# Kernel tuning notes

Hardware: AMD Instinct MI355X
Metric: run time of the kernel (lower is better)

The kernel has to match this reference:

```python
import jax, jax.numpy as jnp
import numpy as np

DIM = 384
HEADS = 12
WS = 7
MLPH = 1536
B = 32
EPS = 1e-5


def _rel_index():
    coords = np.stack(np.meshgrid(np.arange(WS), np.arange(WS), indexing='ij'))  # [2,7,7]
    cf = coords.reshape(2, -1)  # [2,49]
    rel = cf[:, :, None] - cf[:, None, :]  # [2,49,49]
    rel = rel.transpose(1, 2, 0).astype(np.int64)
    rel[:, :, 0] += WS - 1
    rel[:, :, 1] += WS - 1
    rel[:, :, 0] *= 2 * WS - 1
    return jnp.asarray(rel.sum(-1), dtype=jnp.int32)  # [49,49]


def setup_inputs() -> dict:
    key = jax.random.key(0)
    ks = jax.random.split(key, 16)
    H, W = 56, 56
    L = H * W
    s = 0.02
    inp = {
        'x': jax.random.normal(ks[0], (B, L, DIM), jnp.float32),
        'ln1_g': jnp.ones((DIM,), jnp.float32),
        'ln1_b': jnp.zeros((DIM,), jnp.float32),
        'qkv_w': jax.random.normal(ks[1], (DIM, 3 * DIM), jnp.float32) * s,
        'qkv_b': jnp.zeros((3 * DIM,), jnp.float32),
        'rpb_table': jax.random.normal(ks[2], ((2 * WS - 1) ** 2, HEADS), jnp.float32) * s,
        'proj_w': jax.random.normal(ks[3], (DIM, DIM), jnp.float32) * s,
        'proj_b': jnp.zeros((DIM,), jnp.float32),
        'ln2_g': jnp.ones((DIM,), jnp.float32),
        'ln2_b': jnp.zeros((DIM,), jnp.float32),
        'mlp_w1': jax.random.normal(ks[4], (DIM, MLPH), jnp.float32) * s,
        'mlp_b1': jnp.zeros((MLPH,), jnp.float32),
        'mlp_w2': jax.random.normal(ks[5], (MLPH, DIM), jnp.float32) * s,
        'mlp_b2': jnp.zeros((DIM,), jnp.float32),
        'rel_idx': _rel_index(),
        'H': H,
        'W': W,
    }
    return inp


def _ln(x, g, b):
    m = jnp.mean(x, axis=-1, keepdims=True)
    v = jnp.mean(jnp.square(x - m), axis=-1, keepdims=True)
    return (x - m) * jax.lax.rsqrt(v + EPS) * g + b


def reference(x, ln1_g, ln1_b, qkv_w, qkv_b, rpb_table, proj_w, proj_b,
              ln2_g, ln2_b, mlp_w1, mlp_b1, mlp_w2, mlp_b2, rel_idx, H, W):
    Bb, L, C = x.shape
    N = WS * WS
    hd = C // HEADS
    scale = hd ** -0.5

    shortcut = x
    h = _ln(x, ln1_g, ln1_b).reshape(Bb, H, W, C)
    # window partition -> [nW, 49, C]
    h = h.reshape(Bb, H // WS, WS, W // WS, WS, C).transpose(0, 1, 3, 2, 4, 5)
    wins = h.reshape(-1, N, C)
    nW = wins.shape[0]

    qkv = (wins @ qkv_w + qkv_b).reshape(nW, N, 3, HEADS, hd).transpose(2, 0, 3, 1, 4)
    q, k, v = qkv[0] * scale, qkv[1], qkv[2]  # [nW, heads, 49, hd]

    attn = jnp.einsum('bhnd,bhmd->bhnm', q, k)
    bias = rpb_table[rel_idx].transpose(2, 0, 1)  # [heads,49,49]
    attn = jax.nn.softmax(attn + bias[None], axis=-1)
    out = jnp.einsum('bhnm,bhmd->bhnd', attn, v).transpose(0, 2, 1, 3).reshape(nW, N, C)
    out = out @ proj_w + proj_b

    # window reverse -> [B, L, C]
    out = out.reshape(Bb, H // WS, W // WS, WS, WS, C).transpose(0, 1, 3, 2, 4, 5).reshape(Bb, L, C)

    x = shortcut + out
    h2 = _ln(x, ln2_g, ln2_b)
    mlp = jax.nn.gelu(h2 @ mlp_w1 + mlp_b1, approximate=False) @ mlp_w2 + mlp_b2
    return x + mlp
```

## Files before the change

### kernel.cpp

```cpp
#include <hip/hip_runtime.h>
#include <hip/hip_bf16.h>
#include <cstdint>
#include <cstddef>

#define HEADS 12
#define LL 3136
#define ROWS 100352
#define SCALE 0.17677669529663687f

typedef __hip_bfloat16 bf16;
typedef __attribute__((ext_vector_type(8))) short short8;
typedef __attribute__((ext_vector_type(4))) short s4;
typedef __attribute__((ext_vector_type(4))) float f32x4;

__device__ __forceinline__ float bf2f(unsigned short u) {
  union { uint32_t u32; float f; } x; x.u32 = ((uint32_t)u) << 16; return x.f;
}
__device__ __forceinline__ unsigned short f2bf_bits(float f) {
  union { float f; uint32_t u; } x; x.f = f;
  uint32_t r = x.u + 0x7fffu + ((x.u >> 16) & 1u);
  return (unsigned short)(r >> 16);
}
__device__ __forceinline__ float gelu_fast(float x) {
  float t2 = x * (1.5957691216f + 0.0713548162726f * x * x);
  float e = __expf(t2);
  return x * (e / (e + 1.0f));
}

__global__ __launch_bounds__(64) void prep_fragB(const float* __restrict__ src,
    bf16* __restrict__ dst, int K, int N, int scaleLim, float scale) {
  const int nf = blockIdx.x, kf = blockIdx.y;
  const int l = threadIdx.x;
  const int n = nf * 16 + (l & 15);
  const int k0 = kf * 32 + (l >> 4) * 8;
  const float sc = (n < scaleLim) ? scale : 1.f;
  short8 v;
  #pragma unroll
  for (int j = 0; j < 8; ++j)
    v[j] = (short)f2bf_bits(src[(size_t)(k0 + j) * N + n] * sc);
  *(short8*)&dst[(((size_t)nf * (K >> 5) + kf) * 64 + l) * 8] = v;
}

__global__ void prep_qb(const float* __restrict__ qkv_b, float* __restrict__ qb) {
  int idx = blockIdx.x * 256 + threadIdx.x;
  if (idx < 1152) qb[idx] = qkv_b[idx] * (idx < 384 ? SCALE : 1.0f);
}

__global__ void prep_biasM(const float* __restrict__ rpb, const int* __restrict__ rel,
                           f32x4* __restrict__ biasM) {
  int h = blockIdx.x;
  int t = blockIdx.y;
  int mi = t >> 2, ni = t & 3;
  int lane = threadIdx.x;
  int q = ni * 16 + (lane & 15);
  int g = lane >> 4;
  f32x4 v;
  #pragma unroll
  for (int j = 0; j < 4; ++j) {
    int k = mi * 16 + g * 4 + j;
    float b;
    if (k < 49) b = (q < 49) ? rpb[rel[q * 49 + k] * HEADS + h] : 0.f;
    else        b = -1e30f;
    v[j] = b;
  }
  biasM[((h * 4 + mi) * 4 + ni) * 64 + lane] = v;
}

template<bool WIN, bool BF16IN>
__global__ __launch_bounds__(256) void ln_kernel(const float* __restrict__ xf,
    const bf16* __restrict__ xb, const float* __restrict__ g,
    const float* __restrict__ b, bf16* __restrict__ out) {
  int row = blockIdx.x * 4 + (threadIdx.x >> 6);
  int lane = threadIdx.x & 63;
  size_t src;
  if (WIN) {
    int w = row / 49, p = row - w * 49;
    int bb = w >> 6, wy = (w >> 3) & 7, wx = w & 7;
    int iy = p / 7, ix = p - iy * 7;
    int l = (wy * 7 + iy) * 56 + wx * 7 + ix;
    src = ((size_t)bb * LL + l) * 384;
  } else {
    src = (size_t)row * 384;
  }
  float vals[6];
  float s = 0.f, s2 = 0.f;
  #pragma unroll
  for (int j = 0; j < 6; ++j) {
    float v = BF16IN ? bf2f(*(const unsigned short*)&xb[src + lane + 64 * j])
                     : xf[src + lane + 64 * j];
    vals[j] = v; s += v; s2 += v * v;
  }
  #pragma unroll
  for (int off = 32; off >= 1; off >>= 1) {
    s  += __shfl_xor(s, off);
    s2 += __shfl_xor(s2, off);
  }
  float m  = s * (1.f / 384.f);
  float var = s2 * (1.f / 384.f) - m * m;
  float rs = rsqrtf(var + 1e-5f);
  bf16* orow = out + (size_t)row * 384;
  #pragma unroll
  for (int j = 0; j < 6; ++j) {
    int c = lane + 64 * j;
    orow[c] = __float2bfloat16((vals[j] - m) * rs * g[c] + b[c]);
  }
}

template<int EPI, int KTOT>
__global__ __launch_bounds__(256) void gemm_bt(const bf16* __restrict__ A,
    const bf16* __restrict__ Bt, const float* __restrict__ bias,
    bf16* __restrict__ Cb, float* __restrict__ Cf, const float* __restrict__ resid,
    const bf16* __restrict__ residb, int M, int N) {
  constexpr int KC  = 384;
  constexpr int NCH = KTOT / KC;
  constexpr int NT  = KC / 32;
  constexpr int NKF = KTOT >> 5;
  __shared__ bf16 lsA[128 * KC];
  const int t = threadIdx.x;
  const int lane = t & 63;
  const int wave = t >> 6;
  const int wm = wave >> 1, wn = wave & 1;
  const int lrow = lane & 15;
  const int lk = (lane >> 4) * 8;
  const int nbx = N >> 7;
  const int nwg = (M >> 7) * nbx;
  const int cpx = nwg >> 3;
  const int id2 = (blockIdx.x & 7) * cpx + (blockIdx.x >> 3);
  const int n0 = (id2 % nbx) * 128;
  const int m0 = (id2 / nbx) * 128;

  f32x4 acc[4][4];
  #pragma unroll
  for (int i = 0; i < 4; ++i)
    #pragma unroll
    for (int j = 0; j < 4; ++j) acc[i][j] = (f32x4){0.f, 0.f, 0.f, 0.f};

  for (int kc = 0; kc < NCH; ++kc) {
    if (kc) __syncthreads();
    #pragma unroll
    for (int tt = 0; tt < NT; ++tt) {
      #pragma unroll
      for (int i = 0; i < 2; ++i) {
        int e = (i * 256 + t) * 8;
        int r = e >> 5, c = e & 31;
        const bf16* ga = A + (size_t)(m0 + r) * KTOT + kc * KC + tt * 32 + c;
        __builtin_amdgcn_global_load_lds((const __attribute__((address_space(1))) void*)ga,
            (__attribute__((address_space(3))) void*)&lsA[tt * 4096 + e], 16, 0, 0);
      }
    }
    __syncthreads();
    #pragma unroll
    for (int tt = 0; tt < NT; ++tt) {
      const int kf = kc * NT + tt;
      short8 bfr[4];
      const bf16* fb = Bt + (((size_t)((n0 >> 4) + wn * 4) * NKF + kf) * 64 + lane) * 8;
      #pragma unroll
      for (int ni = 0; ni < 4; ++ni)
        bfr[ni] = *(const short8*)(fb + (size_t)ni * NKF * 512);
      short8 af[4];
      #pragma unroll
      for (int mi = 0; mi < 4; ++mi)
        af[mi] = *(const short8*)&lsA[tt * 4096 + (wm * 64 + mi * 16 + lrow) * 32 + lk];
      #pragma unroll
      for (int mi = 0; mi < 4; ++mi)
        #pragma unroll
        for (int ni = 0; ni < 4; ++ni)
          acc[mi][ni] = __builtin_amdgcn_mfma_f32_16x16x32_bf16(af[mi], bfr[ni], acc[mi][ni], 0, 0, 0);
    }
  }

  #pragma unroll
  for (int mi = 0; mi < 4; ++mi) {
    #pragma unroll
    for (int ni = 0; ni < 4; ++ni) {
      int col = n0 + wn * 64 + ni * 16 + lrow;
      float bv = bias[col];
      #pragma unroll
      for (int j = 0; j < 4; ++j) {
        int row = m0 + wm * 64 + mi * 16 + (lane >> 4) * 4 + j;
        float v = acc[mi][ni][j] + bv;
        if constexpr (EPI == 0) {
          Cb[(size_t)row * N + col] = __float2bfloat16(v);
        } else if constexpr (EPI == 1) {
          Cb[(size_t)row * N + col] = __float2bfloat16(gelu_fast(v));
        } else if constexpr (EPI == 2) {
          int w = row / 49, p = row - w * 49;
          int bb = w >> 6, wy = (w >> 3) & 7, wx = w & 7;
          int iy = p / 7, ix = p - iy * 7;
          int l = (wy * 7 + iy) * 56 + wx * 7 + ix;
          size_t di = ((size_t)bb * LL + l) * 384 + col;
          Cb[di] = __float2bfloat16(v + resid[di]);
        } else {
          size_t di = (size_t)row * N + col;
          Cf[di] = v + bf2f(*(const unsigned short*)&residb[di]);
        }
      }
    }
  }
}

__global__ __launch_bounds__(256) void attn_mfma(const bf16* __restrict__ qkv,
    const f32x4* __restrict__ biasM, bf16* __restrict__ out) {
  __shared__ __align__(16) short lds4[4][6272];
  const int wv = threadIdx.x >> 6;
  const int lane = threadIdx.x & 63;
  const int w = blockIdx.x * 4 + wv;
  const int h = blockIdx.y;
  short* L = &lds4[wv][0];
  const short* base = (const short*)(qkv + (size_t)w * 49 * 1152 + h * 32);

  #pragma unroll
  for (int i = 0; i < 4; ++i) {
    int t = i * 64 + lane;
    int r = t >> 2, c = t & 3;
    short8 qv, kv, vv;
    if (r < 49) {
      const short* rp = base + (size_t)r * 1152;
      qv = *(const short8*)(rp + c * 8);
      kv = *(const short8*)(rp + 384 + c * 8);
      vv = *(const short8*)(rp + 768 + c * 8);
    } else {
      qv = (short8)0; kv = (short8)0; vv = (short8)0;
    }
    *(short8*)&L[r * 32 + c * 8] = kv;
    *(short8*)&L[2048 + r * 32 + c * 8] = qv;
    #pragma unroll
    for (int j = 0; j < 8; ++j) L[4096 + (c * 8 + j) * 68 + r] = vv[j];
  }

  const int g = lane >> 4, r15 = lane & 15;

  short8 ka[4], qb[4];
  #pragma unroll
  for (int mi = 0; mi < 4; ++mi)
    ka[mi] = *(const short8*)&L[(mi * 16 + r15) * 32 + g * 8];
  #pragma unroll
  for (int ni = 0; ni < 4; ++ni)
    qb[ni] = *(const short8*)&L[2048 + (ni * 16 + r15) * 32 + g * 8];

  f32x4 sT[4][4];
  #pragma unroll
  for (int mi = 0; mi < 4; ++mi)
    #pragma unroll
    for (int ni = 0; ni < 4; ++ni)
      sT[mi][ni] = biasM[((h * 4 + mi) * 4 + ni) * 64 + lane];
  #pragma unroll
  for (int mi = 0; mi < 4; ++mi)
    #pragma unroll
    for (int ni = 0; ni < 4; ++ni)
      sT[mi][ni] = __builtin_amdgcn_mfma_f32_16x16x32_bf16(ka[mi], qb[ni], sT[mi][ni], 0, 0, 0);

  float inv_[4];
  #pragma unroll
  for (int ni = 0; ni < 4; ++ni) {
    float m = -1e30f;
    #pragma unroll
    for (int mi = 0; mi < 4; ++mi)
      #pragma unroll
      for (int j = 0; j < 4; ++j) m = fmaxf(m, sT[mi][ni][j]);
    m = fmaxf(m, __shfl_xor(m, 16));
    m = fmaxf(m, __shfl_xor(m, 32));
    float s = 0.f;
    #pragma unroll
    for (int mi = 0; mi < 4; ++mi)
      #pragma unroll
      for (int j = 0; j < 4; ++j) {
        float p = __expf(sT[mi][ni][j] - m);
        sT[mi][ni][j] = p; s += p;
      }
    s += __shfl_xor(s, 16);
    s += __shfl_xor(s, 32);
    inv_[ni] = 1.f / s;
  }

  s4 pa[4][4];
  #pragma unroll
  for (int mi = 0; mi < 4; ++mi)
    #pragma unroll
    for (int ni = 0; ni < 4; ++ni) {
      s4 p;
      #pragma unroll
      for (int j = 0; j < 4; ++j)
        p[j] = (short)f2bf_bits(sT[mi][ni][j] * inv_[ni]);
      pa[mi][ni] = p;
    }

  s4 vb[4][2];
  #pragma unroll
  for (int mi = 0; mi < 4; ++mi)
    #pragma unroll
    for (int di = 0; di < 2; ++di)
      vb[mi][di] = *(const s4*)&L[4096 + (di * 16 + r15) * 68 + mi * 16 + g * 4];

  f32x4 o[4][2];
  #pragma unroll
  for (int ni = 0; ni < 4; ++ni)
    #pragma unroll
    for (int di = 0; di < 2; ++di) o[ni][di] = (f32x4){0.f, 0.f, 0.f, 0.f};

  asm volatile("s_nop 3" ::: );
  #pragma unroll
  for (int ni = 0; ni < 4; ++ni)
    #pragma unroll
    for (int di = 0; di < 2; ++di)
      #pragma unroll
      for (int mi = 0; mi < 4; ++mi) {
#if __has_builtin(__builtin_amdgcn_mfma_f32_16x16x16bf16_1k)
        o[ni][di] = __builtin_amdgcn_mfma_f32_16x16x16bf16_1k(pa[mi][ni], vb[mi][di], o[ni][di], 0, 0, 0);
#else
        asm volatile("v_mfma_f32_16x16x16_bf16 %0, %1, %2, %0"
                     : "+v"(o[ni][di]) : "v"(pa[mi][ni]), "v"(vb[mi][di]));
#endif
      }
  asm volatile("s_nop 7\n\ts_nop 7" ::: );

  bf16* op = out + ((size_t)w * 49) * 384 + h * 32;
  #pragma unroll
  for (int ni = 0; ni < 4; ++ni)
    #pragma unroll
    for (int di = 0; di < 2; ++di)
      #pragma unroll
      for (int j = 0; j < 4; ++j) {
        int q = ni * 16 + g * 4 + j;
        if (q < 49)
          op[(size_t)q * 384 + di * 16 + r15] = __float2bfloat16(o[ni][di][j]);
      }
}

extern "C" void kernel_launch(void* const* d_in, const int* in_sizes, int n_in,
                              void* d_out, int out_size, void* d_ws, size_t ws_size,
                              hipStream_t stream) {
  const float* x      = (const float*)d_in[0];
  const float* ln1_g  = (const float*)d_in[1];
  const float* ln1_b  = (const float*)d_in[2];
  const float* qkv_w  = (const float*)d_in[3];
  const float* qkv_b  = (const float*)d_in[4];
  const float* rpb    = (const float*)d_in[5];
  const float* proj_w = (const float*)d_in[6];
  const float* proj_b = (const float*)d_in[7];
  const float* ln2_g  = (const float*)d_in[8];
  const float* ln2_b  = (const float*)d_in[9];
  const float* mlp_w1 = (const float*)d_in[10];
  const float* mlp_b1 = (const float*)d_in[11];
  const float* mlp_w2 = (const float*)d_in[12];
  const float* mlp_b2 = (const float*)d_in[13];
  const int*   rel    = (const int*)d_in[14];

  char* ws = (char*)d_ws;
  const size_t OFF_WQKV  = 0;
  const size_t OFF_WPROJ = OFF_WQKV + (size_t)1152 * 384 * 2;
  const size_t OFF_WM1   = OFF_WPROJ + (size_t)384 * 384 * 2;
  const size_t OFF_WM2   = OFF_WM1 + (size_t)1536 * 384 * 2;
  const size_t OFF_QB    = OFF_WM2 + (size_t)384 * 1536 * 2;
  const size_t OFF_HWIN  = 3659776;
  const size_t OFF_QKV   = OFF_HWIN + (size_t)ROWS * 384 * 2;
  const size_t OFF_ATTN  = OFF_QKV + (size_t)ROWS * 1152 * 2;
  const size_t OFF_X2    = OFF_ATTN + (size_t)ROWS * 384 * 2;
  const size_t OFF_M1    = OFF_QKV;
  const size_t OFF_H2    = OFF_HWIN;
  const size_t OFF_BIASM = OFF_X2 + (size_t)ROWS * 384 * 2;

  bf16*  wqkv  = (bf16*)(ws + OFF_WQKV);
  bf16*  wproj = (bf16*)(ws + OFF_WPROJ);
  bf16*  wm1   = (bf16*)(ws + OFF_WM1);
  bf16*  wm2   = (bf16*)(ws + OFF_WM2);
  float* qb    = (float*)(ws + OFF_QB);
  f32x4* biasM = (f32x4*)(ws + OFF_BIASM);
  bf16*  hwin  = (bf16*)(ws + OFF_HWIN);
  bf16*  qkvb  = (bf16*)(ws + OFF_QKV);
  bf16*  attnb = (bf16*)(ws + OFF_ATTN);
  bf16*  x2b   = (bf16*)(ws + OFF_X2);
  bf16*  m1    = (bf16*)(ws + OFF_M1);
  bf16*  h2    = (bf16*)(ws + OFF_H2);
  float* outp  = (float*)d_out;

  prep_fragB<<<dim3(1152 / 16, 384 / 32), 64, 0, stream>>>(qkv_w, wqkv, 384, 1152, 384, SCALE);
  prep_fragB<<<dim3(384 / 16, 384 / 32), 64, 0, stream>>>(proj_w, wproj, 384, 384, 0, 1.f);
  prep_fragB<<<dim3(1536 / 16, 384 / 32), 64, 0, stream>>>(mlp_w1, wm1, 384, 1536, 0, 1.f);
  prep_fragB<<<dim3(384 / 16, 1536 / 32), 64, 0, stream>>>(mlp_w2, wm2, 1536, 384, 0, 1.f);
  prep_qb<<<5, 256, 0, stream>>>(qkv_b, qb);
  prep_biasM<<<dim3(12, 16), 64, 0, stream>>>(rpb, rel, biasM);

  ln_kernel<true, false><<<ROWS / 4, 256, 0, stream>>>(x, nullptr, ln1_g, ln1_b, hwin);
  gemm_bt<0, 384><<<(1152 / 128) * (ROWS / 128), 256, 0, stream>>>(
      hwin, wqkv, qb, qkvb, nullptr, nullptr, nullptr, ROWS, 1152);
  attn_mfma<<<dim3(512, HEADS), 256, 0, stream>>>(qkvb, biasM, attnb);
  gemm_bt<2, 384><<<(384 / 128) * (ROWS / 128), 256, 0, stream>>>(
      attnb, wproj, proj_b, x2b, nullptr, x, nullptr, ROWS, 384);
  ln_kernel<false, true><<<ROWS / 4, 256, 0, stream>>>(nullptr, x2b, ln2_g, ln2_b, h2);
  gemm_bt<1, 384><<<(1536 / 128) * (ROWS / 128), 256, 0, stream>>>(
      h2, wm1, mlp_b1, m1, nullptr, nullptr, nullptr, ROWS, 1536);
  gemm_bt<3, 1536><<<(384 / 128) * (ROWS / 128), 256, 0, stream>>>(
      m1, wm2, mlp_b2, nullptr, outp, nullptr, x2b, ROWS, 384);
}
```

Measured before the change: 1.073 ms.

## Store GEMM A operands in MFMA fragment layout and drop LDS staging

```diff
diff --git a/kernel.cpp b/kernel.cpp
--- a/kernel.cpp
+++ b/kernel.cpp
@@ -25,6 +25,10 @@
   float t2 = x * (1.5957691216f + 0.0713548162726f * x * x);
   float e = __expf(t2);
   return x * (e / (e + 1.0f));
+}
+__device__ __forceinline__ size_t frag_addr(int row, int c, int nkf) {
+  return ((size_t)(row >> 4) * nkf + (c >> 5)) * 512
+       + (size_t)(((row & 15) + (((c & 31) >> 3) << 4)) * 8 + (c & 7));
 }
 
 __global__ __launch_bounds__(64) void prep_fragB(const float* __restrict__ src,
@@ -98,30 +102,25 @@
   float m  = s * (1.f / 384.f);
   float var = s2 * (1.f / 384.f) - m * m;
   float rs = rsqrtf(var + 1e-5f);
-  bf16* orow = out + (size_t)row * 384;
   #pragma unroll
   for (int j = 0; j < 6; ++j) {
     int c = lane + 64 * j;
-    orow[c] = __float2bfloat16((vals[j] - m) * rs * g[c] + b[c]);
+    float v = (vals[j] - m) * rs * g[c] + b[c];
+    out[frag_addr(row, c, 12)] = __float2bfloat16(v);
   }
 }
 
 template<int EPI, int KTOT>
-__global__ __launch_bounds__(256) void gemm_bt(const bf16* __restrict__ A,
-    const bf16* __restrict__ Bt, const float* __restrict__ bias,
+__global__ __launch_bounds__(256) void gemm_fr(const bf16* __restrict__ Af,
+    const bf16* __restrict__ Bf, const float* __restrict__ bias,
     bf16* __restrict__ Cb, float* __restrict__ Cf, const float* __restrict__ resid,
     const bf16* __restrict__ residb, int M, int N) {
-  constexpr int KC  = 384;
-  constexpr int NCH = KTOT / KC;
-  constexpr int NT  = KC / 32;
   constexpr int NKF = KTOT >> 5;
-  __shared__ bf16 lsA[128 * KC];
   const int t = threadIdx.x;
   const int lane = t & 63;
   const int wave = t >> 6;
   const int wm = wave >> 1, wn = wave & 1;
   const int lrow = lane & 15;
-  const int lk = (lane >> 4) * 8;
   const int nbx = N >> 7;
   const int nwg = (M >> 7) * nbx;
   const int cpx = nwg >> 3;
@@ -129,44 +128,29 @@
   const int n0 = (id2 % nbx) * 128;
   const int m0 = (id2 / nbx) * 128;
 
+  const bf16* fa = Af + (((size_t)(m0 >> 4) + wm * 4) * NKF * 64 + lane) * 8;
+  const bf16* fb = Bf + (((size_t)(n0 >> 4) + wn * 4) * NKF * 64 + lane) * 8;
+
   f32x4 acc[4][4];
   #pragma unroll
   for (int i = 0; i < 4; ++i)
     #pragma unroll
     for (int j = 0; j < 4; ++j) acc[i][j] = (f32x4){0.f, 0.f, 0.f, 0.f};
 
-  for (int kc = 0; kc < NCH; ++kc) {
-    if (kc) __syncthreads();
-    #pragma unroll
-    for (int tt = 0; tt < NT; ++tt) {
-      #pragma unroll
-      for (int i = 0; i < 2; ++i) {
-        int e = (i * 256 + t) * 8;
-        int r = e >> 5, c = e & 31;
-        const bf16* ga = A + (size_t)(m0 + r) * KTOT + kc * KC + tt * 32 + c;
-        __builtin_amdgcn_global_load_lds((const __attribute__((address_space(1))) void*)ga,
-            (__attribute__((address_space(3))) void*)&lsA[tt * 4096 + e], 16, 0, 0);
-      }
-    }
-    __syncthreads();
-    #pragma unroll
-    for (int tt = 0; tt < NT; ++tt) {
-      const int kf = kc * NT + tt;
-      short8 bfr[4];
-      const bf16* fb = Bt + (((size_t)((n0 >> 4) + wn * 4) * NKF + kf) * 64 + lane) * 8;
+  #pragma unroll 4
+  for (int kf = 0; kf < NKF; ++kf) {
+    short8 af[4], bfr[4];
+    #pragma unroll
+    for (int mi = 0; mi < 4; ++mi)
+      af[mi] = *(const short8*)(fa + ((size_t)mi * NKF + kf) * 512);
+    #pragma unroll
+    for (int ni = 0; ni < 4; ++ni)
+      bfr[ni] = *(const short8*)(fb + ((size_t)ni * NKF + kf) * 512);
+    #pragma unroll
+    for (int mi = 0; mi < 4; ++mi)
       #pragma unroll
       for (int ni = 0; ni < 4; ++ni)
-        bfr[ni] = *(const short8*)(fb + (size_t)ni * NKF * 512);
-      short8 af[4];
-      #pragma unroll
-      for (int mi = 0; mi < 4; ++mi)
-        af[mi] = *(const short8*)&lsA[tt * 4096 + (wm * 64 + mi * 16 + lrow) * 32 + lk];
-      #pragma unroll
-      for (int mi = 0; mi < 4; ++mi)
-        #pragma unroll
-        for (int ni = 0; ni < 4; ++ni)
-          acc[mi][ni] = __builtin_amdgcn_mfma_f32_16x16x32_bf16(af[mi], bfr[ni], acc[mi][ni], 0, 0, 0);
-    }
+        acc[mi][ni] = __builtin_amdgcn_mfma_f32_16x16x32_bf16(af[mi], bfr[ni], acc[mi][ni], 0, 0, 0);
   }
 
   #pragma unroll
@@ -182,7 +166,7 @@
         if constexpr (EPI == 0) {
           Cb[(size_t)row * N + col] = __float2bfloat16(v);
         } else if constexpr (EPI == 1) {
-          Cb[(size_t)row * N + col] = __float2bfloat16(gelu_fast(v));
+          Cb[frag_addr(row, col, N >> 5)] = __float2bfloat16(gelu_fast(v));
         } else if constexpr (EPI == 2) {
           int w = row / 49, p = row - w * 49;
           int bb = w >> 6, wy = (w >> 3) & 7, wx = w & 7;
@@ -314,7 +298,6 @@
       }
   asm volatile("s_nop 7\n\ts_nop 7" ::: );
 
-  bf16* op = out + ((size_t)w * 49) * 384 + h * 32;
   #pragma unroll
   for (int ni = 0; ni < 4; ++ni)
     #pragma unroll
@@ -322,8 +305,12 @@
       #pragma unroll
       for (int j = 0; j < 4; ++j) {
         int q = ni * 16 + g * 4 + j;
-        if (q < 49)
-          op[(size_t)q * 384 + di * 16 + r15] = __float2bfloat16(o[ni][di][j]);
+        if (q < 49) {
+          int row = w * 49 + q;
+          size_t ad = ((size_t)(row >> 4) * 12 + h) * 512
+                    + (size_t)(((row & 15) + (di * 2 + (r15 >> 3)) * 16) * 8 + (r15 & 7));
+          out[ad] = __float2bfloat16(o[ni][di][j]);
+        }
       }
 }
 
@@ -382,14 +369,14 @@
   prep_biasM<<<dim3(12, 16), 64, 0, stream>>>(rpb, rel, biasM);
 
   ln_kernel<true, false><<<ROWS / 4, 256, 0, stream>>>(x, nullptr, ln1_g, ln1_b, hwin);
-  gemm_bt<0, 384><<<(1152 / 128) * (ROWS / 128), 256, 0, stream>>>(
+  gemm_fr<0, 384><<<(1152 / 128) * (ROWS / 128), 256, 0, stream>>>(
       hwin, wqkv, qb, qkvb, nullptr, nullptr, nullptr, ROWS, 1152);
   attn_mfma<<<dim3(512, HEADS), 256, 0, stream>>>(qkvb, biasM, attnb);
-  gemm_bt<2, 384><<<(384 / 128) * (ROWS / 128), 256, 0, stream>>>(
+  gemm_fr<2, 384><<<(384 / 128) * (ROWS / 128), 256, 0, stream>>>(
       attnb, wproj, proj_b, x2b, nullptr, x, nullptr, ROWS, 384);
   ln_kernel<false, true><<<ROWS / 4, 256, 0, stream>>>(nullptr, x2b, ln2_g, ln2_b, h2);
-  gemm_bt<1, 384><<<(1536 / 128) * (ROWS / 128), 256, 0, stream>>>(
+  gemm_fr<1, 384><<<(1536 / 128) * (ROWS / 128), 256, 0, stream>>>(
       h2, wm1, mlp_b1, m1, nullptr, nullptr, nullptr, ROWS, 1536);
-  gemm_bt<3, 1536><<<(384 / 128) * (ROWS / 128), 256, 0, stream>>>(
+  gemm_fr<3, 1536><<<(384 / 128) * (ROWS / 128), 256, 0, stream>>>(
       m1, wm2, mlp_b2, nullptr, outp, nullptr, x2b, ROWS, 384);
 }
```

After: 1.124 ms. 1.05x slower.
